# Optimization experiments

Hardware: AMD Instinct MI355X
Metric: run time of the kernel (lower is better)

The kernel has to match this reference:

```python
import jax, jax.numpy as jnp
import numpy as np


def conv1d(x, w, b, pad):
    # x: (B, Cin, T), w: (Cout, Cin, K), b: (Cout,)
    y = jax.lax.conv_general_dilated(x, w, window_strides=(1,), padding=[(pad, pad)],
                                     dimension_numbers=('NCH', 'OIH', 'NCH'))
    return y + b[None, :, None]


def setup_inputs() -> dict:
    key = jax.random.key(0)
    ks = jax.random.split(key, 12)
    B, Cm, T1, Ct, T2, Ca = 8, 80, 800, 512, 200, 80
    queries = jax.random.normal(ks[0], (B, Cm, T1), dtype=jnp.float32)
    keys = jax.random.normal(ks[1], (B, Ct, T2), dtype=jnp.float32)
    query_lens = jnp.full((B,), T1, dtype=jnp.int32)
    key_lens = jax.random.randint(ks[2], (B,), T2 // 2, T2 + 1)
    # mask True where key position is padding (>= key_len): (B, T2, 1)
    mask = (jnp.arange(T2)[None, :] >= key_lens[:, None])[:, :, None]
    attn_prior = jax.random.uniform(ks[3], (B, T1, T2), dtype=jnp.float32) + 0.1
    # key_proj: Conv1d(512->1024, k=3, pad=1) + ReLU + Conv1d(1024->80, k=1)
    kp_w1 = jax.random.normal(ks[4], (2 * Ct, Ct, 3), jnp.float32) * 0.02
    kp_b1 = jnp.zeros((2 * Ct,), jnp.float32)
    kp_w2 = jax.random.normal(ks[5], (Ca, 2 * Ct, 1), jnp.float32) * 0.02
    kp_b2 = jnp.zeros((Ca,), jnp.float32)
    # query_proj (3xconv): Conv1d(80->160,k3)+ReLU+Conv1d(160->80,k1)+ReLU+Conv1d(80->80,k1)
    qp_w1 = jax.random.normal(ks[6], (2 * Cm, Cm, 3), jnp.float32) * 0.05
    qp_b1 = jnp.zeros((2 * Cm,), jnp.float32)
    qp_w2 = jax.random.normal(ks[7], (Cm, 2 * Cm, 1), jnp.float32) * 0.05
    qp_b2 = jnp.zeros((Cm,), jnp.float32)
    qp_w3 = jax.random.normal(ks[8], (Ca, Cm, 1), jnp.float32) * 0.05
    qp_b3 = jnp.zeros((Ca,), jnp.float32)
    return {"queries": queries, "keys": keys, "query_lens": query_lens, "mask": mask,
            "attn_prior": attn_prior, "kp_w1": kp_w1, "kp_b1": kp_b1, "kp_w2": kp_w2,
            "kp_b2": kp_b2, "qp_w1": qp_w1, "qp_b1": qp_b1, "qp_w2": qp_w2,
            "qp_b2": qp_b2, "qp_w3": qp_w3, "qp_b3": qp_b3}


def reference(queries, keys, query_lens, mask, attn_prior,
              kp_w1, kp_b1, kp_w2, kp_b2,
              qp_w1, qp_b1, qp_w2, qp_b2, qp_w3, qp_b3):
    # key projection: (B, Ct, T2) -> (B, Ca, T2)
    ke = conv1d(keys, kp_w1, kp_b1, pad=1)
    ke = jax.nn.relu(ke)
    ke = conv1d(ke, kp_w2, kp_b2, pad=0)
    # query projection ('3xconv'): (B, Cm, T1) -> (B, Ca, T1)
    qe = conv1d(queries, qp_w1, qp_b1, pad=1)
    qe = jax.nn.relu(qe)
    qe = conv1d(qe, qp_w2, qp_b2, pad=0)
    qe = jax.nn.relu(qe)
    qe = conv1d(qe, qp_w3, qp_b3, pad=0)
    # broadcasted squared L2 distance: (B, Ca, T1, T2) -> reduce C -> (B, 1, T1, T2)
    diff2 = (qe[:, :, :, None] - ke[:, :, None, :]) ** 2
    attn = -0.0005 * jnp.sum(diff2, axis=1, keepdims=True)
    # prior in log domain
    attn = jax.nn.log_softmax(attn, axis=3) + jnp.log(attn_prior[:, None] + 1e-8)
    attn_logprob = attn
    # mask (B, T2, 1) -> (B, 1, 1, T2)
    m = jnp.transpose(mask, (0, 2, 1))[:, :, None, :]
    attn = jnp.where(m, -jnp.inf, attn)
    attn = jax.nn.softmax(attn, axis=3)
    return (attn, attn_logprob)
```

## Files before the change

### kernel.cpp

```cpp
#include <hip/hip_runtime.h>
#include <hip/hip_bf16.h>
#include <math.h>

#define B_  8
#define CM  80
#define T1_ 800
#define CT  512
#define T2_ 200
#define CA  80

using bf16 = __hip_bfloat16;
typedef __attribute__((ext_vector_type(8))) short bf16x8;
typedef __attribute__((ext_vector_type(4))) float f32x4;

#define LDSW 56
#define LDSW2 72
#define LDSW3 168
#define LDSW4 104

__device__ __forceinline__ float load_sel(const void* p, long idx, int isf32) {
  if (isf32) return ((const float*)p)[idx];
  return __bfloat162float(((const bf16*)p)[idx]);
}

__device__ __forceinline__ unsigned short f2bf(float x) {
  bf16 h = __float2bfloat16(x);
  return *reinterpret_cast<unsigned short*>(&h);
}

__device__ __forceinline__ int detect_f32(const unsigned short* q) {
  __shared__ int s_f;
  const int tid = threadIdx.x;
  if (tid < 64) {
    unsigned short u = q[2 * tid];
    int e = (u >> 7) & 0xFF;
    unsigned long long bal = __ballot(e < 100 || e > 154);
    if (tid == 0) s_f = (__popcll(bal) >= 16) ? 1 : 0;
  }
  __syncthreads();
  return s_f;
}

__device__ void task_cvt_t(const void* X, bf16* XT, int f, int C, int T,
                           int id2, int tilesT, float* smem, int tid) {
  const int per_b = tilesT * ((C + 31) >> 5);
  const int b = id2 / per_b;
  const int r = id2 - b * per_b;
  const int ct = r / tilesT, tt = r - ct * tilesT;
  const int c0 = ct * 32, t0 = tt * 32;
  const int tx = tid & 31, trow = tid >> 5;
#pragma unroll
  for (int p = 0; p < 4; ++p) {
    const int cr = trow + 8 * p;
    if (c0 + cr < C && t0 + tx < T)
      smem[cr * 33 + tx] = load_sel(X, ((long)b * C + c0 + cr) * T + t0 + tx, f);
  }
  __syncthreads();
#pragma unroll
  for (int p = 0; p < 4; ++p) {
    const int tr = trow + 8 * p;
    if (t0 + tr < T && c0 + tx < C)
      XT[((long)b * T + t0 + tr) * C + c0 + tx] =
          __float2bfloat16(smem[tx * 33 + tr]);
  }
}

__device__ void task_wt3v(const void* W, bf16* WT, int f, int Co, int Ci,
                          int id2, int tid) {
  const int i = id2 * 256 + tid;
  const int g4 = Ci >> 2;
  if (i >= Co * g4) return;
  const int co = i / g4, ci = (i - co * g4) * 4;
  const long sbase = ((long)co * Ci + ci) * 3;
  float w[12];
  if (f) {
    const float4* s = (const float4*)((const float*)W + sbase);
    float4 f0 = s[0], f1 = s[1], f2 = s[2];
    w[0]=f0.x; w[1]=f0.y; w[2]=f0.z; w[3]=f0.w; w[4]=f1.x; w[5]=f1.y;
    w[6]=f1.z; w[7]=f1.w; w[8]=f2.x; w[9]=f2.y; w[10]=f2.z; w[11]=f2.w;
  } else {
#pragma unroll
    for (int j = 0; j < 12; ++j) w[j] = load_sel(W, sbase + j, 0);
  }
#pragma unroll
  for (int dk = 0; dk < 3; ++dk) {
    ushort4 u;
    u.x = f2bf(w[0 * 3 + dk]); u.y = f2bf(w[1 * 3 + dk]);
    u.z = f2bf(w[2 * 3 + dk]); u.w = f2bf(w[3 * 3 + dk]);
    *(ushort4*)(WT + ((long)dk * Co + co) * Ci + ci) = u;
  }
}

__device__ void task_cvtv(const void* W, bf16* O, int f, int n, int id2, int tid) {
  const int i = (id2 * 256 + tid) * 4;
  if (i >= n) return;
  ushort4 u;
  if (f) {
    float4 v = *(const float4*)((const float*)W + i);
    u.x = f2bf(v.x); u.y = f2bf(v.y); u.z = f2bf(v.z); u.w = f2bf(v.w);
  } else {
    u.x = f2bf(load_sel(W, i, 0));     u.y = f2bf(load_sel(W, i + 1, 0));
    u.z = f2bf(load_sel(W, i + 2, 0)); u.w = f2bf(load_sel(W, i + 3, 0));
  }
  *(ushort4*)(O + i) = u;
}

__global__ __launch_bounds__(256) void k_prep(
    const void* __restrict__ queries, const void* __restrict__ keys,
    const void* __restrict__ mask,
    const void* __restrict__ kp_w1, const void* __restrict__ kp_b1,
    const void* __restrict__ kp_w2, const void* __restrict__ kp_b2,
    const void* __restrict__ qp_w1, const void* __restrict__ qp_b1,
    const void* __restrict__ qp_w2, const void* __restrict__ qp_b2,
    const void* __restrict__ qp_w3, const void* __restrict__ qp_b3,
    bf16* __restrict__ keysT, bf16* __restrict__ queriesT,
    bf16* __restrict__ w1T, bf16* __restrict__ qw1T,
    bf16* __restrict__ kw2c, bf16* __restrict__ qw2c, bf16* __restrict__ qw3c,
    float* __restrict__ biasf, float* __restrict__ mf) {
  __shared__ float smem[32 * 33];
  const int tid = threadIdx.x;
  const int f = detect_f32((const unsigned short*)queries);
  int id = blockIdx.x;

  if (id < 896) { task_cvt_t(keys, keysT, f, CT, T2_, id, 7, smem, tid); return; }
  id -= 896;
  if (id < 600) { task_cvt_t(queries, queriesT, f, CM, T1_, id, 25, smem, tid); return; }
  id -= 600;
  if (id < 512) { task_wt3v(kp_w1, w1T, f, 1024, CT, id, tid); return; }
  id -= 512;
  if (id < 13) { task_wt3v(qp_w1, qw1T, f, 160, CM, id, tid); return; }
  id -= 13;
  if (id < 80) { task_cvtv(kp_w2, kw2c, f, 80 * 1024, id, tid); return; }
  id -= 80;
  if (id < 13) { task_cvtv(qp_w2, qw2c, f, 80 * 160, id, tid); return; }
  id -= 13;
  if (id < 7) { task_cvtv(qp_w3, qw3c, f, 80 * 80, id, tid); return; }
  id -= 7;

  if (id == 0) {
    for (int i = tid; i < 1424; i += 256) {
      float v;
      if (i < 1024)      v = load_sel(kp_b1, i, f);
      else if (i < 1104) v = load_sel(kp_b2, i - 1024, f);
      else if (i < 1264) v = load_sel(qp_b1, i - 1104, f);
      else if (i < 1344) v = load_sel(qp_b2, i - 1264, f);
      else               v = load_sel(qp_b3, i - 1344, f);
      biasf[i] = v;
    }
    return;
  }

  {
    int* s_fmt = (int*)smem;
    const int nmask = B_ * T2_;
    if (tid == 0) s_fmt[0] = 1;
    __syncthreads();
    const unsigned int* wi = (const unsigned int*)mask;
    const int nw = nmask / 4;
    int pri = 0;
    for (int i = tid; i < nw; i += 256) {
      unsigned int w = wi[i];
      if (w == 0u || w == 1u) continue;
      if (w == 0x3F803F80u || w == 0x00003F80u) { pri = max(pri, 2); continue; }
      if (w == 0x3F800000u) continue;
      unsigned int b0 = w & 0xFFu, b1 = (w >> 8) & 0xFFu,
                   b2 = (w >> 16) & 0xFFu, b3 = (w >> 24) & 0xFFu;
      if (b0 <= 1u && b1 <= 1u && b2 <= 1u && b3 <= 1u) pri = max(pri, 3);
      else pri = max(pri, 2);
    }
    if (pri) atomicMax(&s_fmt[0], pri);
    __syncthreads();
    const int fmt = s_fmt[0];
    for (int i = tid; i < nmask; i += 256) {
      int m;
      if (fmt == 3)      m = ((const unsigned char*)mask)[i] != 0;
      else if (fmt == 2) m = ((const unsigned short*)mask)[i] != 0;
      else               m = (wi[i] != 0u);
      mf[i] = (float)m;
    }
  }
}

__device__ void conv_tile(
    const bf16* __restrict__ XT, const bf16* __restrict__ WT,
    const float* __restrict__ bias, void* __restrict__ Y,
    int Cin, int Cout, int T, int KW, int pad, int relu, int outmode,
    int m0, int n0, short* As, short* Bs) {
  const int K = Cin * KW;
  const int tid = threadIdx.x;
  const int wave = tid >> 6;
  const int lane = tid & 63;

  const int row = tid >> 2;
  const int koff = (tid & 3) * 8;
  const int n = n0 + row;
  const int bb = n / T;
  const int t = n - bb * T;

  const int wm = (wave >> 1) * 32;
  const int wn = (wave & 1) * 32;
  const int fm = lane & 15;
  const int quad = lane >> 4;

  f32x4 acc[2][2] = {};

  const short* ap0 = As + (wm + fm) * LDSW + quad * 8;
  const short* bp0 = Bs + (wn + fm) * LDSW + quad * 8;

  for (int k0 = 0; k0 < K; k0 += 32) {
    {
      const int k = k0 + koff;
      const int m = m0 + row;
      uint4 v = {0u, 0u, 0u, 0u};
      if (m < Cout && k < K) {
        const int dk = k / Cin;
        const int ci = k - dk * Cin;
        v = *(const uint4*)(WT + ((long)dk * Cout + m) * Cin + ci);
      }
      *(uint4*)(As + row * LDSW + koff) = v;
    }
    {
      const int k = k0 + koff;
      uint4 v = {0u, 0u, 0u, 0u};
      if (k < K) {
        const int dk = k / Cin;
        const int ci = k - dk * Cin;
        const int tt = t + dk - pad;
        if (tt >= 0 && tt < T)
          v = *(const uint4*)(XT + ((long)bb * T + tt) * Cin + ci);
      }
      *(uint4*)(Bs + row * LDSW + koff) = v;
    }
    __syncthreads();
    {
      bf16x8 a0 = *(const bf16x8*)(ap0);
      bf16x8 a1 = *(const bf16x8*)(ap0 + 16 * LDSW);
      bf16x8 b0 = *(const bf16x8*)(bp0);
      bf16x8 b1 = *(const bf16x8*)(bp0 + 16 * LDSW);
      acc[0][0] = __builtin_amdgcn_mfma_f32_16x16x32_bf16(a0, b0, acc[0][0], 0, 0, 0);
      acc[0][1] = __builtin_amdgcn_mfma_f32_16x16x32_bf16(a0, b1, acc[0][1], 0, 0, 0);
      acc[1][0] = __builtin_amdgcn_mfma_f32_16x16x32_bf16(a1, b0, acc[1][0], 0, 0, 0);
      acc[1][1] = __builtin_amdgcn_mfma_f32_16x16x32_bf16(a1, b1, acc[1][1], 0, 0, 0);
    }
    __syncthreads();
  }

#pragma unroll
  for (int mi = 0; mi < 2; ++mi) {
    const int mrow = m0 + wm + mi * 16 + quad * 4;
    if (mrow >= Cout) continue;
    float bi[4];
#pragma unroll
    for (int r = 0; r < 4; ++r) bi[r] = bias[mrow + r];
#pragma unroll
    for (int ni = 0; ni < 2; ++ni) {
      const int ncol = n0 + wn + ni * 16 + fm;
      const long base = (long)ncol * Cout + mrow;
      float o[4];
#pragma unroll
      for (int r = 0; r < 4; ++r) {
        float v = acc[mi][ni][r] + bi[r];
        if (relu) v = fmaxf(v, 0.f);
        o[r] = v;
      }
      if (outmode == 0) {
        ushort4 u;
        u.x = f2bf(o[0]); u.y = f2bf(o[1]); u.z = f2bf(o[2]); u.w = f2bf(o[3]);
        *(ushort4*)((bf16*)Y + base) = u;
      } else {
        *(float4*)((float*)Y + base) = make_float4(o[0], o[1], o[2], o[3]);
      }
    }
  }
}

__device__ void conv_tile64_k1(
    const bf16* __restrict__ XT, const bf16* __restrict__ WT,
    const float* __restrict__ bias, bf16* __restrict__ Y,
    int m0, int n0, short* As, short* Bs) {
  const int Cin = CT, Cout = 1024, T = T2_, K = 1536;
  const int tid = threadIdx.x;
  const int wave = tid >> 6;
  const int lane = tid & 63;

  const int row = tid >> 2;
  const int koff = (tid & 3) * 8;
  const int n = n0 + row;
  const int bb = n / T;
  const int t = n - bb * T;

  const int wm = (wave >> 1) * 32;
  const int wn = (wave & 1) * 32;
  const int fm = lane & 15;
  const int quad = lane >> 4;

  f32x4 acc[2][2] = {};

  const short* ap0 = As + (wm + fm) * LDSW2 + quad * 8;
  const short* bp0 = Bs + (wn + fm) * LDSW2 + quad * 8;

  for (int k0 = 0; k0 < K; k0 += 64) {
#pragma unroll
    for (int h = 0; h < 2; ++h) {
      const int k = k0 + h * 32 + koff;
      const int dk = k / Cin;
      const int ci = k - dk * Cin;
      {
        uint4 v = *(const uint4*)(WT + ((long)dk * Cout + m0 + row) * Cin + ci);
        *(uint4*)(As + row * LDSW2 + h * 32 + koff) = v;
      }
      {
        const int tt = t + dk - 1;
        uint4 v = {0u, 0u, 0u, 0u};
        if (tt >= 0 && tt < T)
          v = *(const uint4*)(XT + ((long)bb * T + tt) * Cin + ci);
        *(uint4*)(Bs + row * LDSW2 + h * 32 + koff) = v;
      }
    }
    __syncthreads();
#pragma unroll
    for (int h = 0; h < 2; ++h) {
      bf16x8 a0 = *(const bf16x8*)(ap0 + h * 32);
      bf16x8 a1 = *(const bf16x8*)(ap0 + 16 * LDSW2 + h * 32);
      bf16x8 b0 = *(const bf16x8*)(bp0 + h * 32);
      bf16x8 b1 = *(const bf16x8*)(bp0 + 16 * LDSW2 + h * 32);
      acc[0][0] = __builtin_amdgcn_mfma_f32_16x16x32_bf16(a0, b0, acc[0][0], 0, 0, 0);
      acc[0][1] = __builtin_amdgcn_mfma_f32_16x16x32_bf16(a0, b1, acc[0][1], 0, 0, 0);
      acc[1][0] = __builtin_amdgcn_mfma_f32_16x16x32_bf16(a1, b0, acc[1][0], 0, 0, 0);
      acc[1][1] = __builtin_amdgcn_mfma_f32_16x16x32_bf16(a1, b1, acc[1][1], 0, 0, 0);
    }
    __syncthreads();
  }

#pragma unroll
  for (int mi = 0; mi < 2; ++mi) {
    const int mrow = m0 + wm + mi * 16 + quad * 4;
    float bi[4];
#pragma unroll
    for (int r = 0; r < 4; ++r) bi[r] = bias[mrow + r];
#pragma unroll
    for (int ni = 0; ni < 2; ++ni) {
      const int ncol = n0 + wn + ni * 16 + fm;
      const long base = (long)ncol * Cout + mrow;
      ushort4 u;
      u.x = f2bf(fmaxf(acc[mi][ni][0] + bi[0], 0.f));
      u.y = f2bf(fmaxf(acc[mi][ni][1] + bi[1], 0.f));
      u.z = f2bf(fmaxf(acc[mi][ni][2] + bi[2], 0.f));
      u.w = f2bf(fmaxf(acc[mi][ni][3] + bi[3], 0.f));
      *(ushort4*)(Y + base) = u;
    }
  }
}

__global__ __launch_bounds__(256) void k_conv1(
    const bf16* __restrict__ keysT, const bf16* __restrict__ w1T,
    const float* __restrict__ b_k1, bf16* __restrict__ ke1T,
    const bf16* __restrict__ queriesT, const bf16* __restrict__ qw1T,
    const float* __restrict__ b_q1, bf16* __restrict__ qe1T) {
  __shared__ __align__(16) short sA[64 * LDSW2];
  __shared__ __align__(16) short sB[64 * LDSW2];
  int j = blockIdx.x;
  if (j < 400) {
    conv_tile64_k1(keysT, w1T, b_k1, ke1T, (j / 25) * 64, (j % 25) * 64, sA, sB);
  } else {
    j -= 400;
    conv_tile(queriesT, qw1T, b_q1, qe1T, CM, 160, T1_, 3, 1, 1, 0,
              (j / 100) * 64, (j % 100) * 64, sA, sB);
  }
}

__device__ void conv23_tile(
    const bf16* __restrict__ qe1T, const bf16* __restrict__ qw2c,
    const float* __restrict__ b_q2, const bf16* __restrict__ qw3c,
    const float* __restrict__ b_q3, float* __restrict__ qeT,
    int n0, short* smem) {
  short* sIn = smem;
  short* sW2 = smem + 64 * LDSW3;
  short* sC  = smem;
  short* sW3 = smem + 64 * LDSW3;
  const int tid = threadIdx.x;
  const int wave = tid >> 6;
  const int lane = tid & 63;
  const int fm = lane & 15;
  const int quad = lane >> 4;

#pragma unroll
  for (int c = tid; c < 1280; c += 256) {
    const int row = c / 20, kc = (c - row * 20) * 8;
    uint4 v = *(const uint4*)(qe1T + (long)(n0 + row) * 160 + kc);
    *(uint4*)(sIn + row * LDSW3 + kc) = v;
  }
  for (int c = tid; c < 1600; c += 256) {
    const int row = c / 20, kc = (c - row * 20) * 8;
    uint4 v = *(const uint4*)(qw2c + (long)row * 160 + kc);
    *(uint4*)(sW2 + row * LDSW3 + kc) = v;
  }
  __syncthreads();

  f32x4 acc1[5] = {};
#pragma unroll
  for (int ks = 0; ks < 5; ++ks) {
    bf16x8 b = *(const bf16x8*)(sIn + (16 * wave + fm) * LDSW3 + ks * 32 + quad * 8);
#pragma unroll
    for (int mt = 0; mt < 5; ++mt) {
      bf16x8 a = *(const bf16x8*)(sW2 + (16 * mt + fm) * LDSW3 + ks * 32 + quad * 8);
      acc1[mt] = __builtin_amdgcn_mfma_f32_16x16x32_bf16(a, b, acc1[mt], 0, 0, 0);
    }
  }
  __syncthreads();

#pragma unroll
  for (int mt = 0; mt < 5; ++mt) {
    const int ch = 16 * mt + quad * 4;
    const float4 b2 = *(const float4*)(b_q2 + ch);
    ushort4 u;
    u.x = f2bf(fmaxf(acc1[mt][0] + b2.x, 0.f));
    u.y = f2bf(fmaxf(acc1[mt][1] + b2.y, 0.f));
    u.z = f2bf(fmaxf(acc1[mt][2] + b2.z, 0.f));
    u.w = f2bf(fmaxf(acc1[mt][3] + b2.w, 0.f));
    *(ushort4*)(sC + (16 * wave + fm) * LDSW4 + ch) = u;
  }
  if (tid < 128) {
    const int row = tid >> 1, off = 80 + (tid & 1) * 8;
    uint4 z = {0u, 0u, 0u, 0u};
    *(uint4*)(sC + row * LDSW4 + off) = z;
  }
  for (int c = tid; c < 800; c += 256) {
    const int row = c / 10, kc = (c - row * 10) * 8;
    uint4 v = *(const uint4*)(qw3c + (long)row * 80 + kc);
    *(uint4*)(sW3 + row * LDSW4 + kc) = v;
  }
  if (tid < 160) {
    const int row = tid >> 1, off = 80 + (tid & 1) * 8;
    uint4 z = {0u, 0u, 0u, 0u};
    *(uint4*)(sW3 + row * LDSW4 + off) = z;
  }
  __syncthreads();

  f32x4 acc2[5] = {};
#pragma unroll
  for (int ks = 0; ks < 3; ++ks) {
    bf16x8 b = *(const bf16x8*)(sC + (16 * wave + fm) * LDSW4 + ks * 32 + quad * 8);
#pragma unroll
    for (int mt = 0; mt < 5; ++mt) {
      bf16x8 a = *(const bf16x8*)(sW3 + (16 * mt + fm) * LDSW4 + ks * 32 + quad * 8);
      acc2[mt] = __builtin_amdgcn_mfma_f32_16x16x32_bf16(a, b, acc2[mt], 0, 0, 0);
    }
  }

  const int pos = n0 + 16 * wave + fm;
#pragma unroll
  for (int mt = 0; mt < 5; ++mt) {
    const int ch = 16 * mt + quad * 4;
    const float4 b3 = *(const float4*)(b_q3 + ch);
    float4 o = make_float4(acc2[mt][0] + b3.x, acc2[mt][1] + b3.y,
                           acc2[mt][2] + b3.z, acc2[mt][3] + b3.w);
    *(float4*)(qeT + (long)pos * CA + ch) = o;
  }
}

__global__ __launch_bounds__(256) void k_conv2f(
    const bf16* __restrict__ ke1T, const bf16* __restrict__ kw2c,
    const float* __restrict__ b_k2, float* __restrict__ keT,
    const bf16* __restrict__ qe1T, const bf16* __restrict__ qw2c,
    const float* __restrict__ b_q2, const bf16* __restrict__ qw3c,
    const float* __restrict__ b_q3, float* __restrict__ qeT) {
  __shared__ __align__(16) short smem[64 * LDSW3 + 80 * LDSW3];
  int j = blockIdx.x;
  if (j < 50) {
    conv_tile(ke1T, kw2c, b_k2, keT, 1024, CA, T2_, 1, 0, 0, 1,
              (j / 25) * 64, (j % 25) * 64, smem, smem + 64 * LDSW);
  } else {
    conv23_tile(qe1T, qw2c, b_q2, qw3c, b_q3, qeT, (j - 50) * 64, smem);
  }
}

__global__ __launch_bounds__(256) void k_dist(
    const float* __restrict__ qeT, const float* __restrict__ keT,
    const void* __restrict__ prior, const float* __restrict__ mf,
    void* __restrict__ out, const unsigned short* __restrict__ qprobe) {
  __shared__ float sq[4 * CA];
  __shared__ float redA[16], redB[16], redC[16], redD[16];
  const int f = detect_f32(qprobe);
  const int b = blockIdx.y;
  const int t1base = blockIdx.x * 4;
  const int tid = threadIdx.x;
  const int wid = tid >> 6;

  for (int i = tid; i < 4 * CA; i += 256) {
    int u = i / CA, c = i - u * CA;
    sq[i] = qeT[((long)b * T1_ + t1base + u) * CA + c];
  }
  __syncthreads();

  const int t2 = tid;
  const bool valid = (t2 < T2_);
  float x[4] = {-INFINITY, -INFINITY, -INFINITY, -INFINITY};
  if (valid) {
    const float4* kb = (const float4*)(keT + ((long)b * T2_ + t2) * CA);
    float s[4] = {0.f, 0.f, 0.f, 0.f};
#pragma unroll 4
    for (int j = 0; j < CA / 4; ++j) {
      float4 kv = kb[j];
#pragma unroll
      for (int u = 0; u < 4; ++u) {
        float4 qv = ((const float4*)(sq + u * CA))[j];
        float d;
        d = qv.x - kv.x; s[u] = fmaf(d, d, s[u]);
        d = qv.y - kv.y; s[u] = fmaf(d, d, s[u]);
        d = qv.z - kv.z; s[u] = fmaf(d, d, s[u]);
        d = qv.w - kv.w; s[u] = fmaf(d, d, s[u]);
      }
    }
#pragma unroll
    for (int u = 0; u < 4; ++u) x[u] = -0.0005f * s[u];
  }

  const float mval = valid ? mf[b * T2_ + t2] : 0.f;
  const long N = (long)B_ * T1_ * T2_;

  float m[4] = {x[0], x[1], x[2], x[3]};
#pragma unroll
  for (int o = 32; o > 0; o >>= 1)
#pragma unroll
    for (int u = 0; u < 4; ++u) m[u] = fmaxf(m[u], __shfl_down(m[u], o, 64));
  if ((tid & 63) == 0)
#pragma unroll
    for (int u = 0; u < 4; ++u) redA[wid * 4 + u] = m[u];
  __syncthreads();
  float M1[4];
#pragma unroll
  for (int u = 0; u < 4; ++u)
    M1[u] = fmaxf(fmaxf(redA[u], redA[4 + u]), fmaxf(redA[8 + u], redA[12 + u]));

  float e[4], s1[4];
#pragma unroll
  for (int u = 0; u < 4; ++u) {
    e[u] = (x[u] == -INFINITY) ? 0.f : expf(x[u] - M1[u]);
    s1[u] = e[u];
  }
#pragma unroll
  for (int o = 32; o > 0; o >>= 1)
#pragma unroll
    for (int u = 0; u < 4; ++u) s1[u] += __shfl_down(s1[u], o, 64);
  if ((tid & 63) == 0)
#pragma unroll
    for (int u = 0; u < 4; ++u) redB[wid * 4 + u] = s1[u];
  __syncthreads();
  float lp[4];
#pragma unroll
  for (int u = 0; u < 4; ++u) {
    const float S1 = redB[u] + redB[4 + u] + redB[8 + u] + redB[12 + u];
    const float logZ = logf(S1);
    lp[u] = -INFINITY;
    if (valid) {
      const long oidx = ((long)b * T1_ + t1base + u) * T2_ + t2;
      float pr = load_sel(prior, oidx, f);
      lp[u] = (x[u] - M1[u] - logZ) + logf(fmaxf(pr, 0.f) + 1e-8f);
      if (f) ((float*)out)[N + oidx] = lp[u];
      else   ((bf16*)out)[N + oidx] = __float2bfloat16(lp[u]);
    }
  }

  float xm[4], m2[4];
#pragma unroll
  for (int u = 0; u < 4; ++u) {
    xm[u] = (valid && mval != 0.f) ? -INFINITY : lp[u];
    m2[u] = xm[u];
  }
#pragma unroll
  for (int o = 32; o > 0; o >>= 1)
#pragma unroll
    for (int u = 0; u < 4; ++u) m2[u] = fmaxf(m2[u], __shfl_down(m2[u], o, 64));
  if ((tid & 63) == 0)
#pragma unroll
    for (int u = 0; u < 4; ++u) redC[wid * 4 + u] = m2[u];
  __syncthreads();
  float M2[4];
#pragma unroll
  for (int u = 0; u < 4; ++u)
    M2[u] = fmaxf(fmaxf(redC[u], redC[4 + u]), fmaxf(redC[8 + u], redC[12 + u]));

  float e2[4], s2[4];
#pragma unroll
  for (int u = 0; u < 4; ++u) {
    e2[u] = (xm[u] == -INFINITY) ? 0.f : expf(xm[u] - M2[u]);
    s2[u] = e2[u];
  }
#pragma unroll
  for (int o = 32; o > 0; o >>= 1)
#pragma unroll
    for (int u = 0; u < 4; ++u) s2[u] += __shfl_down(s2[u], o, 64);
  if ((tid & 63) == 0)
#pragma unroll
    for (int u = 0; u < 4; ++u) redD[wid * 4 + u] = s2[u];
  __syncthreads();
#pragma unroll
  for (int u = 0; u < 4; ++u) {
    const float S2 = redD[u] + redD[4 + u] + redD[8 + u] + redD[12 + u];
    if (valid) {
      float a = (S2 > 0.f) ? (e2[u] / S2) : 0.f;
      const long oidx = ((long)b * T1_ + t1base + u) * T2_ + t2;
      if (f) ((float*)out)[oidx] = a;
      else   ((bf16*)out)[oidx] = __float2bfloat16(a);
    }
  }
}

extern "C" void kernel_launch(void* const* d_in, const int* in_sizes, int n_in,
                              void* d_out, int out_size, void* d_ws, size_t ws_size,
                              hipStream_t stream) {
  const void* queries = d_in[0];
  const void* keys    = d_in[1];
  const void* mask    = d_in[3];
  const void* prior   = d_in[4];
  const void* kp_w1 = d_in[5];
  const void* kp_b1 = d_in[6];
  const void* kp_w2 = d_in[7];
  const void* kp_b2 = d_in[8];
  const void* qp_w1 = d_in[9];
  const void* qp_b1 = d_in[10];
  const void* qp_w2 = d_in[11];
  const void* qp_b2 = d_in[12];
  const void* qp_w3 = d_in[13];
  const void* qp_b3 = d_in[14];

  float* keT   = (float*)d_ws;
  float* qeT   = keT + 128000;
  float* mf    = qeT + 512000;
  float* biasf = mf + 1600;
  bf16* keysT    = (bf16*)(biasf + 1440);
  bf16* queriesT = keysT + 819200;
  bf16* w1T      = queriesT + 512000;
  bf16* qw1T     = w1T + 1572864;
  bf16* kw2c     = qw1T + 38400;
  bf16* qw2c     = kw2c + 81920;
  bf16* qw3c     = qw2c + 12800;
  bf16* ke1T     = qw3c + 6400;
  bf16* qe1T     = ke1T + 1638400;

  float* b_k1 = biasf;
  float* b_k2 = biasf + 1024;
  float* b_q1 = biasf + 1104;
  float* b_q2 = biasf + 1264;
  float* b_q3 = biasf + 1344;

  k_prep<<<2123, 256, 0, stream>>>(
      queries, keys, mask,
      kp_w1, kp_b1, kp_w2, kp_b2,
      qp_w1, qp_b1, qp_w2, qp_b2, qp_w3, qp_b3,
      keysT, queriesT, w1T, qw1T, kw2c, qw2c, qw3c, biasf, mf);

  k_conv1<<<700, 256, 0, stream>>>(keysT, w1T, b_k1, ke1T,
                                   queriesT, qw1T, b_q1, qe1T);

  k_conv2f<<<150, 256, 0, stream>>>(ke1T, kw2c, b_k2, keT,
                                    qe1T, qw2c, b_q2, qw3c, b_q3, qeT);

  k_dist<<<dim3(200, B_), 256, 0, stream>>>(
      qeT, keT, prior, mf, d_out, (const unsigned short*)queries);
}
```

Baseline: 168.1 us.

## Expand squared distance into dot product plus norms and enlarge key conv tile

The distance kernel now computes ||q||^2 + ||k||^2 - 2 q·k. Query and key norms are produced in the conv epilogues, with the key norm accumulated by atomics, and keys are stored channel-major and pre-scaled by -2 so the inner loop is a single FMA with coalesced loads. The key conv1 GEMM switches to 128x64 tiles with 4x2 MFMA accumulators per wave, cutting the block count and reloads of the key activations. The norm expansion adds cancellation error and makes the key norm depend on float atomic ordering.

New measurement: 167.6 us. Within noise of the previous version (-0.3%).

```diff
diff --git a/kernel.cpp b/kernel.cpp
--- a/kernel.cpp
+++ b/kernel.cpp
@@ -116,7 +116,7 @@
     bf16* __restrict__ keysT, bf16* __restrict__ queriesT,
     bf16* __restrict__ w1T, bf16* __restrict__ qw1T,
     bf16* __restrict__ kw2c, bf16* __restrict__ qw2c, bf16* __restrict__ qw3c,
-    float* __restrict__ biasf, float* __restrict__ mf) {
+    float* __restrict__ biasf, float* __restrict__ mf, float* __restrict__ kn) {
   __shared__ float smem[32 * 33];
   const int tid = threadIdx.x;
   const int f = detect_f32((const unsigned short*)queries);
@@ -147,6 +147,7 @@
       else               v = load_sel(qp_b3, i - 1344, f);
       biasf[i] = v;
     }
+    for (int i = tid; i < B_ * T2_; i += 256) kn[i] = 0.f;
     return;
   }
 
@@ -185,7 +186,7 @@
     const bf16* __restrict__ XT, const bf16* __restrict__ WT,
     const float* __restrict__ bias, void* __restrict__ Y,
     int Cin, int Cout, int T, int KW, int pad, int relu, int outmode,
-    int m0, int n0, short* As, short* Bs) {
+    int m0, int n0, short* As, short* Bs, float* Y2 = nullptr) {
   const int K = Cin * KW;
   const int tid = threadIdx.x;
   const int wave = tid >> 6;
@@ -255,7 +256,6 @@
 #pragma unroll
     for (int ni = 0; ni < 2; ++ni) {
       const int ncol = n0 + wn + ni * 16 + fm;
-      const long base = (long)ncol * Cout + mrow;
       float o[4];
 #pragma unroll
       for (int r = 0; r < 4; ++r) {
@@ -266,15 +266,26 @@
       if (outmode == 0) {
         ushort4 u;
         u.x = f2bf(o[0]); u.y = f2bf(o[1]); u.z = f2bf(o[2]); u.w = f2bf(o[3]);
-        *(ushort4*)((bf16*)Y + base) = u;
+        *(ushort4*)((bf16*)Y + (long)ncol * Cout + mrow) = u;
+      } else if (outmode == 1) {
+        *(float4*)((float*)Y + (long)ncol * Cout + mrow) =
+            make_float4(o[0], o[1], o[2], o[3]);
       } else {
-        *(float4*)((float*)Y + base) = make_float4(o[0], o[1], o[2], o[3]);
+        const int bb2 = ncol / T;
+        const int tloc = ncol - bb2 * T;
+        float s4 = 0.f;
+#pragma unroll
+        for (int r = 0; r < 4; ++r) {
+          ((float*)Y)[((long)bb2 * Cout + mrow + r) * T + tloc] = -2.f * o[r];
+          s4 = fmaf(o[r], o[r], s4);
+        }
+        atomicAdd(&Y2[ncol], s4);
       }
     }
   }
 }
 
-__device__ void conv_tile64_k1(
+__device__ void conv_tile128(
     const bf16* __restrict__ XT, const bf16* __restrict__ WT,
     const float* __restrict__ bias, bf16* __restrict__ Y,
     int m0, int n0, short* As, short* Bs) {
@@ -283,57 +294,64 @@
   const int wave = tid >> 6;
   const int lane = tid & 63;
 
-  const int row = tid >> 2;
-  const int koff = (tid & 3) * 8;
-  const int n = n0 + row;
-  const int bb = n / T;
-  const int t = n - bb * T;
-
-  const int wm = (wave >> 1) * 32;
+  const int rowb = tid >> 2;
+  const int nb = n0 + rowb;
+  const int bbb = nb / T;
+  const int tb = nb - bbb * T;
+
+  const int wm = (wave >> 1) * 64;
   const int wn = (wave & 1) * 32;
   const int fm = lane & 15;
   const int quad = lane >> 4;
 
-  f32x4 acc[2][2] = {};
+  f32x4 acc[4][2] = {};
 
   const short* ap0 = As + (wm + fm) * LDSW2 + quad * 8;
   const short* bp0 = Bs + (wn + fm) * LDSW2 + quad * 8;
 
   for (int k0 = 0; k0 < K; k0 += 64) {
+    const int dk = k0 >> 9;
+    const int ci0 = k0 & 511;
+    {
+      const int arow = tid >> 1;
+      const bf16* src = WT + ((long)dk * Cout + m0 + arow) * Cin + ci0 + (tid & 1) * 32;
+      short* dst = As + arow * LDSW2 + (tid & 1) * 32;
+#pragma unroll
+      for (int hh = 0; hh < 4; ++hh)
+        *(uint4*)(dst + hh * 8) = *(const uint4*)(src + hh * 8);
+    }
+    {
+      const int tt = tb + dk - 1;
+      const int kc0 = (tid & 3) * 16;
+      if (tt >= 0 && tt < T) {
+        const bf16* src = XT + ((long)bbb * T + tt) * Cin + ci0 + kc0;
+        short* dst = Bs + rowb * LDSW2 + kc0;
+        *(uint4*)(dst) = *(const uint4*)(src);
+        *(uint4*)(dst + 8) = *(const uint4*)(src + 8);
+      } else {
+        uint4 z = {0u, 0u, 0u, 0u};
+        short* dst = Bs + rowb * LDSW2 + kc0;
+        *(uint4*)(dst) = z;
+        *(uint4*)(dst + 8) = z;
+      }
+    }
+    __syncthreads();
 #pragma unroll
     for (int h = 0; h < 2; ++h) {
-      const int k = k0 + h * 32 + koff;
-      const int dk = k / Cin;
-      const int ci = k - dk * Cin;
-      {
-        uint4 v = *(const uint4*)(WT + ((long)dk * Cout + m0 + row) * Cin + ci);
-        *(uint4*)(As + row * LDSW2 + h * 32 + koff) = v;
-      }
-      {
-        const int tt = t + dk - 1;
-        uint4 v = {0u, 0u, 0u, 0u};
-        if (tt >= 0 && tt < T)
-          v = *(const uint4*)(XT + ((long)bb * T + tt) * Cin + ci);
-        *(uint4*)(Bs + row * LDSW2 + h * 32 + koff) = v;
-      }
-    }
-    __syncthreads();
-#pragma unroll
-    for (int h = 0; h < 2; ++h) {
-      bf16x8 a0 = *(const bf16x8*)(ap0 + h * 32);
-      bf16x8 a1 = *(const bf16x8*)(ap0 + 16 * LDSW2 + h * 32);
       bf16x8 b0 = *(const bf16x8*)(bp0 + h * 32);
       bf16x8 b1 = *(const bf16x8*)(bp0 + 16 * LDSW2 + h * 32);
-      acc[0][0] = __builtin_amdgcn_mfma_f32_16x16x32_bf16(a0, b0, acc[0][0], 0, 0, 0);
-      acc[0][1] = __builtin_amdgcn_mfma_f32_16x16x32_bf16(a0, b1, acc[0][1], 0, 0, 0);
-      acc[1][0] = __builtin_amdgcn_mfma_f32_16x16x32_bf16(a1, b0, acc[1][0], 0, 0, 0);
-      acc[1][1] = __builtin_amdgcn_mfma_f32_16x16x32_bf16(a1, b1, acc[1][1], 0, 0, 0);
+#pragma unroll
+      for (int mi = 0; mi < 4; ++mi) {
+        bf16x8 a = *(const bf16x8*)(ap0 + mi * 16 * LDSW2 + h * 32);
+        acc[mi][0] = __builtin_amdgcn_mfma_f32_16x16x32_bf16(a, b0, acc[mi][0], 0, 0, 0);
+        acc[mi][1] = __builtin_amdgcn_mfma_f32_16x16x32_bf16(a, b1, acc[mi][1], 0, 0, 0);
+      }
     }
     __syncthreads();
   }
 
 #pragma unroll
-  for (int mi = 0; mi < 2; ++mi) {
+  for (int mi = 0; mi < 4; ++mi) {
     const int mrow = m0 + wm + mi * 16 + quad * 4;
     float bi[4];
 #pragma unroll
@@ -357,15 +375,15 @@
     const float* __restrict__ b_k1, bf16* __restrict__ ke1T,
     const bf16* __restrict__ queriesT, const bf16* __restrict__ qw1T,
     const float* __restrict__ b_q1, bf16* __restrict__ qe1T) {
-  __shared__ __align__(16) short sA[64 * LDSW2];
+  __shared__ __align__(16) short sA[128 * LDSW2];
   __shared__ __align__(16) short sB[64 * LDSW2];
   int j = blockIdx.x;
-  if (j < 400) {
-    conv_tile64_k1(keysT, w1T, b_k1, ke1T, (j / 25) * 64, (j % 25) * 64, sA, sB);
+  if (j < 200) {
+    conv_tile128(keysT, w1T, b_k1, ke1T, (j / 25) * 128, (j % 25) * 64, sA, sB);
   } else {
-    j -= 400;
+    j -= 200;
     conv_tile(queriesT, qw1T, b_q1, qe1T, CM, 160, T1_, 3, 1, 1, 0,
-              (j / 100) * 64, (j % 100) * 64, sA, sB);
+              (j / 100) * 64, (j % 100) * 64, sA, sA + 64 * LDSW);
   }
 }
 
@@ -373,7 +391,7 @@
     const bf16* __restrict__ qe1T, const bf16* __restrict__ qw2c,
     const float* __restrict__ b_q2, const bf16* __restrict__ qw3c,
     const float* __restrict__ b_q3, float* __restrict__ qeT,
-    int n0, short* smem) {
+    float* __restrict__ qn, int n0, short* smem) {
   short* sIn = smem;
   short* sW2 = smem + 64 * LDSW3;
   short* sC  = smem;
@@ -449,37 +467,47 @@
   }
 
   const int pos = n0 + 16 * wave + fm;
+  float p = 0.f;
 #pragma unroll
   for (int mt = 0; mt < 5; ++mt) {
     const int ch = 16 * mt + quad * 4;
     const float4 b3 = *(const float4*)(b_q3 + ch);
     float4 o = make_float4(acc2[mt][0] + b3.x, acc2[mt][1] + b3.y,
                            acc2[mt][2] + b3.z, acc2[mt][3] + b3.w);
+    p = fmaf(o.x, o.x, p); p = fmaf(o.y, o.y, p);
+    p = fmaf(o.z, o.z, p); p = fmaf(o.w, o.w, p);
     *(float4*)(qeT + (long)pos * CA + ch) = o;
   }
+  p += __shfl_xor(p, 16, 64);
+  p += __shfl_xor(p, 32, 64);
+  if (quad == 0) qn[pos] = p;
 }
 
 __global__ __launch_bounds__(256) void k_conv2f(
     const bf16* __restrict__ ke1T, const bf16* __restrict__ kw2c,
     const float* __restrict__ b_k2, float* __restrict__ keT,
+    float* __restrict__ kn,
     const bf16* __restrict__ qe1T, const bf16* __restrict__ qw2c,
     const float* __restrict__ b_q2, const bf16* __restrict__ qw3c,
-    const float* __restrict__ b_q3, float* __restrict__ qeT) {
+    const float* __restrict__ b_q3, float* __restrict__ qeT,
+    float* __restrict__ qn) {
   __shared__ __align__(16) short smem[64 * LDSW3 + 80 * LDSW3];
   int j = blockIdx.x;
   if (j < 50) {
-    conv_tile(ke1T, kw2c, b_k2, keT, 1024, CA, T2_, 1, 0, 0, 1,
-              (j / 25) * 64, (j % 25) * 64, smem, smem + 64 * LDSW);
+    conv_tile(ke1T, kw2c, b_k2, keT, 1024, CA, T2_, 1, 0, 0, 2,
+              (j / 25) * 64, (j % 25) * 64, smem, smem + 64 * LDSW, kn);
   } else {
-    conv23_tile(qe1T, qw2c, b_q2, qw3c, b_q3, qeT, (j - 50) * 64, smem);
+    conv23_tile(qe1T, qw2c, b_q2, qw3c, b_q3, qeT, qn, (j - 50) * 64, smem);
   }
 }
 
 __global__ __launch_bounds__(256) void k_dist(
-    const float* __restrict__ qeT, const float* __restrict__ keT,
+    const float* __restrict__ qeT, const float* __restrict__ keT2,
+    const float* __restrict__ kn, const float* __restrict__ qn,
     const void* __restrict__ prior, const float* __restrict__ mf,
     void* __restrict__ out, const unsigned short* __restrict__ qprobe) {
   __shared__ float sq[4 * CA];
+  __shared__ float sqn[4];
   __shared__ float redA[16], redB[16], redC[16], redD[16];
   const int f = detect_f32(qprobe);
   const int b = blockIdx.y;
@@ -491,29 +519,27 @@
     int u = i / CA, c = i - u * CA;
     sq[i] = qeT[((long)b * T1_ + t1base + u) * CA + c];
   }
+  if (tid < 4) sqn[tid] = qn[b * T1_ + t1base + tid];
   __syncthreads();
 
   const int t2 = tid;
   const bool valid = (t2 < T2_);
   float x[4] = {-INFINITY, -INFINITY, -INFINITY, -INFINITY};
   if (valid) {
-    const float4* kb = (const float4*)(keT + ((long)b * T2_ + t2) * CA);
+    const float* kp = keT2 + (long)b * CA * T2_ + t2;
+    const float knv = kn[b * T2_ + t2];
     float s[4] = {0.f, 0.f, 0.f, 0.f};
-#pragma unroll 4
-    for (int j = 0; j < CA / 4; ++j) {
-      float4 kv = kb[j];
-#pragma unroll
-      for (int u = 0; u < 4; ++u) {
-        float4 qv = ((const float4*)(sq + u * CA))[j];
-        float d;
-        d = qv.x - kv.x; s[u] = fmaf(d, d, s[u]);
-        d = qv.y - kv.y; s[u] = fmaf(d, d, s[u]);
-        d = qv.z - kv.z; s[u] = fmaf(d, d, s[u]);
-        d = qv.w - kv.w; s[u] = fmaf(d, d, s[u]);
-      }
-    }
-#pragma unroll
-    for (int u = 0; u < 4; ++u) x[u] = -0.0005f * s[u];
+#pragma unroll 8
+    for (int j = 0; j < CA; ++j) {
+      const float kv = kp[j * T2_];
+      s[0] = fmaf(kv, sq[0 * CA + j], s[0]);
+      s[1] = fmaf(kv, sq[1 * CA + j], s[1]);
+      s[2] = fmaf(kv, sq[2 * CA + j], s[2]);
+      s[3] = fmaf(kv, sq[3 * CA + j], s[3]);
+    }
+#pragma unroll
+    for (int u = 0; u < 4; ++u)
+      x[u] = -0.0005f * (s[u] + sqn[u] + knv);
   }
 
   const float mval = valid ? mf[b * T2_ + t2] : 0.f;
@@ -629,7 +655,9 @@
   float* qeT   = keT + 128000;
   float* mf    = qeT + 512000;
   float* biasf = mf + 1600;
-  bf16* keysT    = (bf16*)(biasf + 1440);
+  float* kn    = biasf + 1440;
+  float* qn    = kn + 1600;
+  bf16* keysT    = (bf16*)(qn + 6400);
   bf16* queriesT = keysT + 819200;
   bf16* w1T      = queriesT + 512000;
   bf16* qw1T     = w1T + 1572864;
@@ -649,14 +677,14 @@
       queries, keys, mask,
       kp_w1, kp_b1, kp_w2, kp_b2,
       qp_w1, qp_b1, qp_w2, qp_b2, qp_w3, qp_b3,
-      keysT, queriesT, w1T, qw1T, kw2c, qw2c, qw3c, biasf, mf);
-
-  k_conv1<<<700, 256, 0, stream>>>(keysT, w1T, b_k1, ke1T,
+      keysT, queriesT, w1T, qw1T, kw2c, qw2c, qw3c, biasf, mf, kn);
+
+  k_conv1<<<500, 256, 0, stream>>>(keysT, w1T, b_k1, ke1T,
                                    queriesT, qw1T, b_q1, qe1T);
 
-  k_conv2f<<<150, 256, 0, stream>>>(ke1T, kw2c, b_k2, keT,
-                                    qe1T, qw2c, b_q2, qw3c, b_q3, qeT);
+  k_conv2f<<<150, 256, 0, stream>>>(ke1T, kw2c, b_k2, keT, kn,
+                                    qe1T, qw2c, b_q2, qw3c, b_q3, qeT, qn);
 
   k_dist<<<dim3(200, B_), 256, 0, stream>>>(
-      qeT, keT, prior, mf, d_out, (const unsigned short*)queries);
-}
+      qeT, keT, kn, qn, prior, mf, d_out, (const unsigned short*)queries);
+}
```
